# Kernel optimization log

Hardware: AMD Instinct MI355X
Metric: run time of the kernel (lower is better)

## Reference

```python
import jax, jax.numpy as jnp
import numpy as np

EPS = 1e-5

def group_norm(x, num_groups, eps=EPS):
    # x: [B, C, H, W]; no affine (matches F.group_norm with weight=None)
    B, C, H, W = x.shape
    xg = x.reshape(B, num_groups, (C // num_groups) * H * W)
    mean = jnp.mean(xg, axis=-1, keepdims=True)
    var = jnp.var(xg, axis=-1, keepdims=True)
    xg = (xg - mean) * jax.lax.rsqrt(var + eps)
    return xg.reshape(B, C, H, W)

def setup_inputs() -> dict:
    key = jax.random.key(0)
    ks = jax.random.split(key, 5)
    B, C, H, W = 32, 256, 32, 32
    # kaiming-uniform-ish scale for linear weights
    bound = 1.0 / np.sqrt(C)
    x = jax.random.normal(ks[0], (B, C, H, W), dtype=jnp.float32)
    WQ = jax.random.uniform(ks[1], (C, C), jnp.float32, -bound, bound)
    WK = jax.random.uniform(ks[2], (C, C), jnp.float32, -bound, bound)
    WV = jax.random.uniform(ks[3], (C, C), jnp.float32, -bound, bound)
    Wo = jax.random.uniform(ks[4], (C, C), jnp.float32, -bound, bound)
    z = jnp.zeros((C,), jnp.float32)
    return {"x": x, "WQ": WQ, "bQ": z, "WK": WK, "bK": z,
            "WV": WV, "bV": z, "Wo": Wo, "bo": z}

def reference(x, WQ, bQ, WK, bK, WV, bV, Wo, bo):
    B, C, H, W = x.shape
    G = min(32, C)
    h = group_norm(x, G)                      # [B,C,H,W]
    h = h.reshape(B, C, H * W).transpose(0, 2, 1)  # [B, S, C], S = H*W
    q = h @ WQ + bQ
    k = h @ WK + bK
    v = h @ WV + bV
    scale = C ** (-0.5)
    attn = jnp.einsum('bsc,btc->bst', q, k) * scale   # [B,S,S]
    attn = jax.nn.softmax(attn, axis=-1)
    o = jnp.einsum('bst,btc->bsc', attn, v)           # [B,S,C]
    o = o @ Wo + bo                                   # output Nin while in [B,S,C]
    o = o.transpose(0, 2, 1).reshape(B, C, H, W)
    return x + o
```

## Files before the change

### kernel.cpp

```cpp
#include <hip/hip_runtime.h>
#include <stdint.h>

#define BB  32
#define CC  256
#define SS  1024
#define GG  32
#define GCH 8
#define EPS 1e-5f

typedef __attribute__((ext_vector_type(8))) short short8;
typedef __attribute__((ext_vector_type(4))) float f32x4;
typedef __attribute__((ext_vector_type(16))) float f32x16;
typedef unsigned short ushort;

__device__ __forceinline__ float bf2f(ushort u){
  union { unsigned int i; float f; } v; v.i = ((unsigned int)u) << 16; return v.f;
}
__device__ __forceinline__ ushort f2bf(float f){
  union { float f; unsigned int i; } v; v.f = f;
  unsigned int r = v.i + 0x7FFFu + ((v.i >> 16) & 1u);
  return (ushort)(r >> 16);
}
__device__ __forceinline__ unsigned int cvt_pk_bf16(float lo, float hi){
  unsigned int r;
  asm("v_cvt_pk_bf16_f32 %0, %1, %2" : "=v"(r) : "v"(lo), "v"(hi));
  return r;
}

typedef __attribute__((address_space(3))) unsigned int lds_uint;
typedef const __attribute__((address_space(1))) unsigned int glob_uint;
__device__ __forceinline__ void ld_lds16(const void* g, void* l){
  __builtin_amdgcn_global_load_lds((glob_uint*)g, (lds_uint*)l, 16, 0, 0);
}

__global__ __launch_bounds__(256) void sniff_k(const unsigned int* __restrict__ xw,
                                               int* __restrict__ flag)
{
  const int tid = threadIdx.x;
  unsigned int w = xw[tid];
  ushort lo = (ushort)(w & 0xFFFFu);
  int e = (lo >> 7) & 0xFF;
  int ok = (lo == 0 || (e >= 100 && e <= 130)) ? 1 : 0;
  __shared__ int cnt;
  if (tid == 0) cnt = 0;
  __syncthreads();
  atomicAdd(&cnt, ok);
  __syncthreads();
  if (tid == 0) *flag = (cnt > 192) ? 1 : 0;
}

__global__ __launch_bounds__(256) void convert_pre(
    const void* w0, const void* w1, const void* w2, const void* w3,
    const void* b0, const void* b1, const void* b2, const void* b3,
    ushort* __restrict__ WT, float* __restrict__ biasF,
    const int* __restrict__ flag)
{
  const int f = *flag;
  const int z = blockIdx.z;
  const float scl = (z == 0) ? 0.0901684400557f : 1.0f;
  const void* wsel = z==0?w0:z==1?w1:z==2?w2:w3;
  ushort* dst = WT + (long long)z * 65536;
  __shared__ ushort t[64][65];
  const int tid = threadIdx.x;
  const int tx = tid & 63, ty = tid >> 6;
  const int r0 = blockIdx.x * 64, c0 = blockIdx.y * 64;
  for (int j = 0; j < 64; j += 4){
    const int idx = (r0+ty+j)*256 + c0+tx;
    float v = f ? bf2f(((const ushort*)wsel)[idx]) : ((const float*)wsel)[idx];
    t[ty+j][tx] = f2bf(v * scl);
  }
  __syncthreads();
  for (int j = 0; j < 64; j += 4) dst[(c0+ty+j)*256 + r0+tx] = t[tx][ty+j];
  if (blockIdx.x == 0 && blockIdx.y == 0){
    const void* bsel = z==0?b0:z==1?b1:z==2?b2:b3;
    float bv = f ? bf2f(((const ushort*)bsel)[tid]) : ((const float*)bsel)[tid];
    biasF[z*256 + tid] = bv * scl;
  }
}

__global__ __launch_bounds__(256) void gn_stats(const void* __restrict__ x,
                                                float* __restrict__ stats,
                                                const int* __restrict__ flag)
{
  const int f = *flag;
  const int g = blockIdx.x, b = blockIdx.y;
  const int tid = threadIdx.x;
  const long long base = ((long long)b * CC + g * GCH) * SS;
  float sum = 0.f, ss = 0.f;
  if (f){
    const ushort* xg = (const ushort*)x + base;
    #pragma unroll
    for (int j = 0; j < 4; j++){
      uint4 u = *(const uint4*)(xg + (j*256 + tid)*8);
      const ushort* e = (const ushort*)&u;
      #pragma unroll
      for (int i = 0; i < 8; i++){ float v = bf2f(e[i]); sum += v; ss += v*v; }
    }
  } else {
    const float* xg = (const float*)x + base;
    #pragma unroll
    for (int j = 0; j < 8; j++){
      float4 v4 = *(const float4*)(xg + (j*256 + tid)*4);
      sum += v4.x+v4.y+v4.z+v4.w;
      ss  += v4.x*v4.x+v4.y*v4.y+v4.z*v4.z+v4.w*v4.w;
    }
  }
  __shared__ float red[8];
  const int lane = tid & 63, w = tid >> 6;
  #pragma unroll
  for (int o = 32; o > 0; o >>= 1){
    sum += __shfl_down(sum, o);
    ss  += __shfl_down(ss, o);
  }
  if (lane == 0){ red[w] = sum; red[4+w] = ss; }
  __syncthreads();
  if (tid == 0){
    float s1 = red[0]+red[1]+red[2]+red[3];
    float s2 = red[4]+red[5]+red[6]+red[7];
    float mean = s1 / (float)(GCH*SS);
    float var  = s2 / (float)(GCH*SS) - mean*mean;
    const int idx = b*GG + g;
    stats[idx*2]   = mean;
    stats[idx*2+1] = rsqrtf(var + EPS);
  }
}

__global__ __launch_bounds__(256) void gn_norm(const void* __restrict__ x,
                                               ushort* __restrict__ h,
                                               const float* __restrict__ stats,
                                               const int* __restrict__ flag)
{
  const int f = *flag;
  const int c0 = blockIdx.x * 64, s0 = blockIdx.y * 64, b = blockIdx.z;
  const int tid = threadIdx.x;
  __shared__ ushort T[64][72];
  const int row = tid >> 2;
  const int qr  = tid & 3;
  const int g = (c0 + row) >> 3;
  const float mean = stats[(b*GG + g)*2];
  const float rstd = stats[(b*GG + g)*2 + 1];
  const long long xrow = ((long long)b * CC + c0 + row) * SS + s0;
  if (f){
    const ushort* xr = (const ushort*)x + xrow;
    #pragma unroll
    for (int j = 0; j < 2; j++){
      const int col = qr*16 + j*8;
      uint4 u = *(const uint4*)(xr + col);
      const ushort* e = (const ushort*)&u;
      #pragma unroll
      for (int i = 0; i < 8; i++) T[row][col+i] = f2bf((bf2f(e[i]) - mean) * rstd);
    }
  } else {
    const float* xr = (const float*)x + xrow;
    #pragma unroll
    for (int j = 0; j < 4; j++){
      const int col = qr*16 + j*4;
      float4 v4 = *(const float4*)(xr + col);
      T[row][col+0] = f2bf((v4.x - mean) * rstd);
      T[row][col+1] = f2bf((v4.y - mean) * rstd);
      T[row][col+2] = f2bf((v4.z - mean) * rstd);
      T[row][col+3] = f2bf((v4.w - mean) * rstd);
    }
  }
  __syncthreads();
  #pragma unroll
  for (int pass = 0; pass < 2; pass++){
    const int sr = pass*32 + (tid >> 3);
    const int cl = (tid & 7) * 8;
    ushort tmp[8];
    #pragma unroll
    for (int e = 0; e < 8; e++) tmp[e] = T[cl+e][sr];
    *(uint4*)(&h[((long long)b * SS + s0 + sr) * CC + c0 + cl]) = *(const uint4*)tmp;
  }
}

template<int MODE>
__global__ __launch_bounds__(256) void gemm128(
    const ushort* __restrict__ A,
    const ushort* __restrict__ BT,
    ushort* __restrict__ Cmat,
    int lda, int ldb, int ldc, int K,
    long long sA, long long sB, long long sC,
    const float* __restrict__ biasF,
    const void* __restrict__ xres,
    void* __restrict__ outp,
    ushort* __restrict__ vTp,
    long long xoff,
    const int* __restrict__ flag)
{
  extern __shared__ __attribute__((aligned(16))) ushort smem[];
  ushort* As = smem;
  ushort* Bs = smem + 5120;
  const int tid  = threadIdx.x;
  const int lane = tid & 63;
  const int w    = tid >> 6;
  const int wr   = w >> 1, wc = w & 1;
  const int bz   = blockIdx.z;
  const int m0 = blockIdx.x * 128;
  const int n0 = blockIdx.y * 128;

  const int srow  = tid >> 1;
  const int shalf = (tid & 1) * 16;

  f32x4 acc[4][4] = {};

  const ushort* Ablk = A + (long long)bz * sA + (long long)(m0 + srow) * lda + shalf;
  const ushort* Bblk = BT + (long long)bz * sB + (long long)(n0 + srow) * ldb + shalf;
  ushort* asw = &As[srow * 40 + shalf];
  ushort* bsw = &Bs[srow * 40 + shalf];

  const int koff = 8 * (lane >> 4);
  const int rr   = lane & 15;

  for (int k0 = 0; k0 < K; k0 += 32){
    uint4 va0 = *(const uint4*)(Ablk + k0);
    uint4 va1 = *(const uint4*)(Ablk + k0 + 8);
    uint4 vb0 = *(const uint4*)(Bblk + k0);
    uint4 vb1 = *(const uint4*)(Bblk + k0 + 8);
    *(uint4*)(asw)     = va0;
    *(uint4*)(asw + 8) = va1;
    *(uint4*)(bsw)     = vb0;
    *(uint4*)(bsw + 8) = vb1;
    __syncthreads();
    short8 af[4], bfr[4];
    #pragma unroll
    for (int mf = 0; mf < 4; mf++)
      af[mf] = *(const short8*)(&As[(wr*64 + mf*16 + rr) * 40 + koff]);
    #pragma unroll
    for (int nf = 0; nf < 4; nf++)
      bfr[nf] = *(const short8*)(&Bs[(wc*64 + nf*16 + rr) * 40 + koff]);
    #pragma unroll
    for (int mf = 0; mf < 4; mf++)
      #pragma unroll
      for (int nf = 0; nf < 4; nf++)
        acc[mf][nf] = __builtin_amdgcn_mfma_f32_16x16x32_bf16(af[mf], bfr[nf], acc[mf][nf], 0, 0, 0);
    __syncthreads();
  }

  const int rb = 4 * (lane >> 4);
  if (MODE == 0){
    if (bz < 2){
      ushort* Co = Cmat + (long long)bz * sC;
      #pragma unroll
      for (int mf = 0; mf < 4; mf++){
        #pragma unroll
        for (int nf = 0; nf < 4; nf++){
          const int col = n0 + wc*64 + nf*16 + rr;
          const float badd = biasF[bz*256 + col];
          #pragma unroll
          for (int r = 0; r < 4; r++){
            const int row = m0 + wr*64 + mf*16 + rb + r;
            Co[(long long)row * ldc + col] = f2bf(acc[mf][nf][r] + badd);
          }
        }
      }
    } else {
      #pragma unroll
      for (int mf = 0; mf < 4; mf++){
        #pragma unroll
        for (int nf = 0; nf < 4; nf++){
          const int col = n0 + wc*64 + nf*16 + rr;
          const float badd = biasF[512 + col];
          #pragma unroll
          for (int r = 0; r < 4; r++){
            const int row = m0 + wr*64 + mf*16 + rb + r;
            const int bL = row >> 10, s = row & 1023;
            vTp[((long long)bL * CC + col) * SS + s] = f2bf(acc[mf][nf][r] + badd);
          }
        }
      }
    }
  } else {
    const int bL = m0 >> 10;
    const int s0 = m0 & 1023;
    #pragma unroll
    for (int mf = 0; mf < 4; mf++){
      #pragma unroll
      for (int nf = 0; nf < 4; nf++){
        const int colL = wc*64 + nf*16 + rr;
        const float badd = biasF[768 + n0 + colL];
        #pragma unroll
        for (int r = 0; r < 4; r++){
          const int rowL = wr*64 + mf*16 + rb + r;
          smem[colL * 128 + rowL] = f2bf(acc[mf][nf][r] + badd);
        }
      }
    }
    __syncthreads();
    const int f = *flag;
    for (int i = tid; i < 2048; i += 256){
      const int colL = i >> 4;
      const int rowL = (i & 15) * 8;
      const long long oi = xoff + ((long long)bL * CC + n0 + colL) * SS + s0 + rowL;
      const ushort* pu = &smem[colL * 128 + rowL];
      if (f){
        const ushort* xu = (const ushort*)xres + oi;
        ushort* ou = (ushort*)outp + oi;
        ushort tmp[8];
        #pragma unroll
        for (int e = 0; e < 8; e++) tmp[e] = f2bf(bf2f(xu[e]) + bf2f(pu[e]));
        *(uint4*)ou = *(const uint4*)tmp;
      } else {
        const float* xf = (const float*)xres + oi;
        float* of = (float*)outp + oi;
        float4 a0 = *(const float4*)xf;
        float4 a1 = *(const float4*)(xf + 4);
        float4 r0, r1;
        r0.x = a0.x + bf2f(pu[0]); r0.y = a0.y + bf2f(pu[1]);
        r0.z = a0.z + bf2f(pu[2]); r0.w = a0.w + bf2f(pu[3]);
        r1.x = a1.x + bf2f(pu[4]); r1.y = a1.y + bf2f(pu[5]);
        r1.z = a1.z + bf2f(pu[6]); r1.w = a1.w + bf2f(pu[7]);
        *(float4*)of = r0;
        *(float4*)(of + 4) = r1;
      }
    }
  }
}

__global__ __launch_bounds__(512, 1) void attn_fused(
    const ushort* __restrict__ q, const ushort* __restrict__ k,
    const ushort* __restrict__ vT, ushort* __restrict__ oC)
{
  __shared__ ushort Kb[2][64 * 256];
  __shared__ ushort Vb[2][256 * 64];
  const int tid = threadIdx.x, lane = tid & 63, w = tid >> 6;
  const int l31 = lane & 31, hi2 = lane >> 5;
  const int qg = w & 3, ch = w >> 2;
  const int b = blockIdx.x, qt = blockIdx.y;

  const char* kgB = (const char*)(k + (long long)b * SS * CC);
  const char* vgB = (const char*)(vT + (long long)b * CC * SS);
  const int qrow = qt*128 + qg*32 + l31;
  const ushort* qgp = q + ((long long)b * SS + qrow) * CC + hi2*8;
  ushort* ogq = oC + ((long long)b * SS + qrow) * CC + ch*128;

  short8 qf[16];
  #pragma unroll
  for (int kk = 0; kk < 16; kk++)
    qf[kk] = *(const short8*)(qgp + kk*16);

  f32x16 Oa[4] = {};
  float mrow = -1e30f, lrow = 0.0f;

  #define STAGE(buf, t0)                                                        \
  {                                                                             \
    _Pragma("unroll")                                                           \
    for (int j = 0; j < 4; j++){                                                \
      const int ck = j*8 + w;                                                   \
      const int tr = ck*2 + (lane >> 5);                                        \
      const int xb = ((lane & 31) * 16) ^ ((tr & 31) << 4);                     \
      ld_lds16(kgB + (long long)((t0) + tr) * 512 + xb, &Kb[buf][ck * 512]);    \
    }                                                                           \
    _Pragma("unroll")                                                           \
    for (int j = 0; j < 4; j++){                                                \
      const int ck = j*8 + w;                                                   \
      const int vr = ck*2 + (lane >> 5);                                        \
      const int u  = (lane & 31) ^ ((vr & 7) << 2);                             \
      const int vc = vr*4 + (u & 3);                                            \
      const int tb = (u >> 2) * 16;                                             \
      ld_lds16(vgB + (long long)vc * 2048 + (t0)*2 + tb, &Vb[buf][ck * 512]);   \
    }                                                                           \
  }

  STAGE(0, 0);
  asm volatile("s_waitcnt vmcnt(0)" ::: "memory");
  __builtin_amdgcn_sched_barrier(0);
  __syncthreads();

  const int coff = hi2 * 16;
  const int kswz = l31 << 4;

  for (int t = 0; t < 16; t++){
    const int cur = t & 1;
    if (t < 15) STAGE(cur ^ 1, (t+1)*64);

    f32x16 Sa0 = {}, Sa1 = {};
    __builtin_amdgcn_s_setprio(1);
    #pragma unroll
    for (int kk = 0; kk < 16; kk++){
      const int off = kk*32 + coff;
      short8 ka0 = *(const short8*)((const char*)&Kb[cur][0] + l31*512 + (off ^ kswz));
      short8 ka1 = *(const short8*)((const char*)&Kb[cur][0] + (32 + l31)*512 + (off ^ kswz));
      Sa0 = __builtin_amdgcn_mfma_f32_32x32x16_bf16(ka0, qf[kk], Sa0, 0, 0, 0);
      Sa1 = __builtin_amdgcn_mfma_f32_32x32x16_bf16(ka1, qf[kk], Sa1, 0, 0, 0);
    }
    __builtin_amdgcn_s_setprio(0);

    float mx = Sa0[0];
    #pragma unroll
    for (int r = 1; r < 16; r++) mx = fmaxf(mx, Sa0[r]);
    #pragma unroll
    for (int r = 0; r < 16; r++) mx = fmaxf(mx, Sa1[r]);
    mx = fmaxf(mx, __shfl_xor(mx, 32));
    if (!__all(mx <= mrow + 8.0f)){
      const float mn = fmaxf(mrow, mx);
      const float sc = __builtin_amdgcn_exp2f(mrow - mn);
      mrow = mn;
      lrow *= sc;
      #pragma unroll
      for (int nf = 0; nf < 4; nf++)
        #pragma unroll
        for (int r = 0; r < 16; r++) Oa[nf][r] *= sc;
    }
    float rs = 0.0f;
    #pragma unroll
    for (int r = 0; r < 16; r++){
      Sa0[r] = __builtin_amdgcn_exp2f(Sa0[r] - mrow); rs += Sa0[r];
      Sa1[r] = __builtin_amdgcn_exp2f(Sa1[r] - mrow); rs += Sa1[r];
    }
    rs += __shfl_xor(rs, 32);
    lrow += rs;

    __builtin_amdgcn_s_setprio(1);
    #pragma unroll
    for (int g = 0; g < 4; g++){
      unsigned int b0, b1, b2, b3;
      if (g < 2){
        b0 = cvt_pk_bf16(Sa0[(g&1)*8+0], Sa0[(g&1)*8+1]);
        b1 = cvt_pk_bf16(Sa0[(g&1)*8+2], Sa0[(g&1)*8+3]);
        b2 = cvt_pk_bf16(Sa0[(g&1)*8+4], Sa0[(g&1)*8+5]);
        b3 = cvt_pk_bf16(Sa0[(g&1)*8+6], Sa0[(g&1)*8+7]);
      } else {
        b0 = cvt_pk_bf16(Sa1[(g&1)*8+0], Sa1[(g&1)*8+1]);
        b1 = cvt_pk_bf16(Sa1[(g&1)*8+2], Sa1[(g&1)*8+3]);
        b2 = cvt_pk_bf16(Sa1[(g&1)*8+4], Sa1[(g&1)*8+5]);
        b3 = cvt_pk_bf16(Sa1[(g&1)*8+6], Sa1[(g&1)*8+7]);
      }
      unsigned int s0 = (unsigned int)__shfl_xor((int)b0, 32);
      unsigned int s1 = (unsigned int)__shfl_xor((int)b1, 32);
      unsigned int s2 = (unsigned int)__shfl_xor((int)b2, 32);
      unsigned int s3 = (unsigned int)__shfl_xor((int)b3, 32);
      union { uint4 u; short8 s; } pw;
      pw.u.x = hi2 ? s2 : b0;
      pw.u.y = hi2 ? s3 : b1;
      pw.u.z = hi2 ? b2 : s0;
      pw.u.w = hi2 ? b3 : s1;
      const short8 pb = pw.s;
      const int G = g*2 + hi2;
      #pragma unroll
      for (int nf = 0; nf < 4; nf++){
        const int c = ch*128 + nf*32 + l31;
        const int vr = c >> 2;
        const int slot = (((G << 2) | (c & 3)) ^ ((vr & 7) << 2));
        short8 va = *(const short8*)((const char*)&Vb[cur][0] + vr*512 + slot*16);
        Oa[nf] = __builtin_amdgcn_mfma_f32_32x32x16_bf16(va, pb, Oa[nf], 0, 0, 0);
      }
    }
    __builtin_amdgcn_s_setprio(0);

    asm volatile("s_waitcnt vmcnt(0)" ::: "memory");
    __builtin_amdgcn_sched_barrier(0);
    __syncthreads();
  }
  #undef STAGE

  const float inv = 1.0f / lrow;
  #pragma unroll
  for (int nf = 0; nf < 4; nf++){
    #pragma unroll
    for (int g = 0; g < 4; g++){
      uint2 ov;
      ov.x = cvt_pk_bf16(Oa[nf][g*4+0] * inv, Oa[nf][g*4+1] * inv);
      ov.y = cvt_pk_bf16(Oa[nf][g*4+2] * inv, Oa[nf][g*4+3] * inv);
      *(uint2*)(ogq + nf*32 + g*8 + hi2*4) = ov;
    }
  }
}

extern "C" void kernel_launch(void* const* d_in, const int* in_sizes, int n_in,
                              void* d_out, int out_size, void* d_ws, size_t ws_size,
                              hipStream_t stream)
{
  (void)in_sizes; (void)n_in; (void)out_size;
  const void* x  = d_in[0];
  const void* WQ = d_in[1];
  const void* bQ = d_in[2];
  const void* WK = d_in[3];
  const void* bK = d_in[4];
  const void* WV = d_in[5];
  const void* bV = d_in[6];
  const void* Wo = d_in[7];
  const void* bo = d_in[8];

  const long long NE  = (long long)BB * SS * CC;
  const long long SC  = (long long)SS * CC;

  uint8_t* base = (uint8_t*)d_ws;
  int* flag          = (int*)base;
  float* biasF       = (float*)(base + 256);
  float* stats       = (float*)(base + 256 + 4096);
  ushort* WT         = (ushort*)(base + 256 + 4096 + 8192);
  ushort* h          = WT + 4 * 65536;

  const long long fixedB = 256 + 4096 + 8192 + 4LL*65536*2 + NE*2;
  int CB = 1;
  for (int c = 32; c >= 1; c >>= 1){
    if (fixedB + 4LL * c * SC * 2 <= (long long)ws_size){ CB = c; break; }
  }

  ushort* q  = h + NE;
  ushort* k  = q + (long long)CB * SC;
  ushort* vT = k + (long long)CB * SC;
  ushort* oC = vT + (long long)CB * SC;

  dim3 blk(256);
  const size_t shmem = 32768;

  sniff_k<<<1, blk, 0, stream>>>((const unsigned int*)x, flag);
  convert_pre<<<dim3(4, 4, 4), blk, 0, stream>>>(WQ, WK, WV, Wo, bQ, bK, bV, bo, WT, biasF, flag);
  gn_stats<<<dim3(GG, BB), blk, 0, stream>>>(x, stats, flag);
  gn_norm<<<dim3(4, 16, BB), blk, 0, stream>>>(x, h, stats, flag);

  for (int c0 = 0; c0 < BB; c0 += CB){
    const ushort* hC = h + (long long)c0 * SC;
    gemm128<0><<<dim3(CB*8, 2, 3), blk, shmem, stream>>>(
        hC, WT, q, CC, CC, CC, CC,
        0LL, 65536LL, (long long)CB * SC,
        biasF, nullptr, nullptr, vT, 0LL, flag);
    attn_fused<<<dim3(CB, 8), dim3(512), 0, stream>>>(q, k, vT, oC);
    gemm128<3><<<dim3(CB*8, 2, 1), blk, shmem, stream>>>(
        oC, WT + 3*65536, nullptr, CC, CC, SS, CC,
        0LL, 0LL, 0LL,
        biasF, x, d_out, nullptr, (long long)c0 * SC, flag);
  }
}
```

Baseline: 157.8 us.

## Use direct global-to-LDS loads with XOR swizzle and K=64 tiles in gemm128

Replaces the register-staged global→LDS copy in the 128x128 GEMM with direct buffer-to-LDS loads (ld_lds16) into an XOR-swizzled layout. It also doubles the K step to 64 so each barrier pair covers two MFMA k-substeps. The aim is to cut VGPR staging, LDS bank conflicts and barrier overhead per unit of work. It uses more shared memory, and it waits on vmcnt(0) with no double buffering, so load latency is still exposed.

```diff
diff --git a/kernel.cpp b/kernel.cpp
--- a/kernel.cpp
+++ b/kernel.cpp
@@ -190,7 +190,7 @@
 {
   extern __shared__ __attribute__((aligned(16))) ushort smem[];
   ushort* As = smem;
-  ushort* Bs = smem + 5120;
+  ushort* Bs = smem + 8192;
   const int tid  = threadIdx.x;
   const int lane = tid & 63;
   const int w    = tid >> 6;
@@ -199,41 +199,55 @@
   const int m0 = blockIdx.x * 128;
   const int n0 = blockIdx.y * 128;
 
-  const int srow  = tid >> 1;
-  const int shalf = (tid & 1) * 16;
+  const int rr = lane & 15;
+  const int hi = lane >> 4;
+  const int crow = lane >> 3;
+  const int pslot = lane & 7;
 
   f32x4 acc[4][4] = {};
 
-  const ushort* Ablk = A + (long long)bz * sA + (long long)(m0 + srow) * lda + shalf;
-  const ushort* Bblk = BT + (long long)bz * sB + (long long)(n0 + srow) * ldb + shalf;
-  ushort* asw = &As[srow * 40 + shalf];
-  ushort* bsw = &Bs[srow * 40 + shalf];
-
-  const int koff = 8 * (lane >> 4);
-  const int rr   = lane & 15;
-
-  for (int k0 = 0; k0 < K; k0 += 32){
-    uint4 va0 = *(const uint4*)(Ablk + k0);
-    uint4 va1 = *(const uint4*)(Ablk + k0 + 8);
-    uint4 vb0 = *(const uint4*)(Bblk + k0);
-    uint4 vb1 = *(const uint4*)(Bblk + k0 + 8);
-    *(uint4*)(asw)     = va0;
-    *(uint4*)(asw + 8) = va1;
-    *(uint4*)(bsw)     = vb0;
-    *(uint4*)(bsw + 8) = vb1;
+  const ushort* Ab = A + (long long)bz * sA;
+  const ushort* Bb = BT + (long long)bz * sB;
+
+  for (int k0 = 0; k0 < K; k0 += 64){
+    #pragma unroll
+    for (int j = 0; j < 4; j++){
+      const int ck = w*4 + j;
+      const int r  = ck*8 + crow;
+      const int s  = pslot ^ (r & 7);
+      ld_lds16(Ab + (long long)(m0 + r) * lda + k0 + s*8, &As[ck * 512]);
+    }
+    #pragma unroll
+    for (int j = 0; j < 4; j++){
+      const int ck = w*4 + j;
+      const int r  = ck*8 + crow;
+      const int s  = pslot ^ (r & 7);
+      ld_lds16(Bb + (long long)(n0 + r) * ldb + k0 + s*8, &Bs[ck * 512]);
+    }
+    asm volatile("s_waitcnt vmcnt(0)" ::: "memory");
+    __builtin_amdgcn_sched_barrier(0);
     __syncthreads();
-    short8 af[4], bfr[4];
-    #pragma unroll
-    for (int mf = 0; mf < 4; mf++)
-      af[mf] = *(const short8*)(&As[(wr*64 + mf*16 + rr) * 40 + koff]);
-    #pragma unroll
-    for (int nf = 0; nf < 4; nf++)
-      bfr[nf] = *(const short8*)(&Bs[(wc*64 + nf*16 + rr) * 40 + koff]);
-    #pragma unroll
-    for (int mf = 0; mf < 4; mf++)
-      #pragma unroll
-      for (int nf = 0; nf < 4; nf++)
-        acc[mf][nf] = __builtin_amdgcn_mfma_f32_16x16x32_bf16(af[mf], bfr[nf], acc[mf][nf], 0, 0, 0);
+
+    #pragma unroll
+    for (int kk = 0; kk < 2; kk++){
+      short8 af[4], bfr[4];
+      const int lbyte = kk*64 + hi*16;
+      #pragma unroll
+      for (int mf = 0; mf < 4; mf++){
+        const int row = wr*64 + mf*16 + rr;
+        af[mf] = *(const short8*)((const char*)As + row*128 + (lbyte ^ ((row & 7) << 4)));
+      }
+      #pragma unroll
+      for (int nf = 0; nf < 4; nf++){
+        const int row = wc*64 + nf*16 + rr;
+        bfr[nf] = *(const short8*)((const char*)Bs + row*128 + (lbyte ^ ((row & 7) << 4)));
+      }
+      #pragma unroll
+      for (int mf = 0; mf < 4; mf++)
+        #pragma unroll
+        for (int nf = 0; nf < 4; nf++)
+          acc[mf][nf] = __builtin_amdgcn_mfma_f32_16x16x32_bf16(af[mf], bfr[nf], acc[mf][nf], 0, 0, 0);
+    }
     __syncthreads();
   }
 
```

New measurement: 151.2 us. 4.2% less time.
